# Performance work log

Measured on AMD Instinct MI355X. Metric: run time of the kernel, lower is better.

Reference implementation:

```python
import jax, jax.numpy as jnp
import numpy as np

B, S, D, H = 8, 1024, 512, 8


def setup_inputs() -> dict:
    key = jax.random.key(0)
    ks = jax.random.split(key, 10)
    sc = 0.05
    return {
        "x": jax.random.normal(ks[0], (B, S, D), dtype=jnp.float32),
        "Wq": jax.random.normal(ks[1], (H, D, D), dtype=jnp.float32) * sc,
        "bq": jax.random.normal(ks[2], (H, D), dtype=jnp.float32) * sc,
        "Wk": jax.random.normal(ks[3], (H, D, D), dtype=jnp.float32) * sc,
        "bk": jax.random.normal(ks[4], (H, D), dtype=jnp.float32) * sc,
        "Wv": jax.random.normal(ks[5], (H, D, D), dtype=jnp.float32) * sc,
        "bv": jax.random.normal(ks[6], (H, D), dtype=jnp.float32) * sc,
        "Wo": jax.random.normal(ks[7], (H * D, D), dtype=jnp.float32) * sc,
        "bo": jax.random.normal(ks[8], (D,), dtype=jnp.float32) * sc,
    }


def reference(x, Wq, bq, Wk, bk, Wv, bv, Wo, bo):
    # Per-head full-dim projections, batched across heads.
    # x: [B,S,D]; Wq/Wk/Wv: [H,D,D]; b*: [H,D]
    q = jnp.einsum('bsd,hde->bhse', x, Wq) + bq[None, :, None, :]
    k = jnp.einsum('bsd,hde->bhse', x, Wk) + bk[None, :, None, :]
    v = jnp.einsum('bsd,hde->bhse', x, Wv) + bv[None, :, None, :]
    d = x.shape[-1]
    scores = jnp.einsum('bhse,bhte->bhst', q, k) / jnp.sqrt(jnp.float32(d))
    attn = jax.nn.softmax(scores, axis=-1)
    heads = jnp.einsum('bhst,bhte->bhse', attn, v)  # [B,H,S,D]
    # concat along feature dim (head order matches torch cat order)
    concat = jnp.transpose(heads, (0, 2, 1, 3)).reshape(x.shape[0], x.shape[1], -1)
    return concat @ Wo + bo
```

## Files before the change

kernel.cpp:

```cpp
#include <hip/hip_runtime.h>
#include <cstdint>
#include <cstddef>

#define BB 8
#define SS 1024
#define DDIM 512
#define HH 8
#define BS 8192
#define HD 4096

typedef __attribute__((ext_vector_type(4))) float f32x4;
typedef __attribute__((ext_vector_type(8))) short bf16x8;
typedef __attribute__((ext_vector_type(4))) unsigned short u16x4;


__device__ __forceinline__ unsigned short f2bf(float f) {
  union { float f; unsigned int u; } x; x.f = f;
  unsigned int r = x.u + 0x7fffu + ((x.u >> 16) & 1u);
  return (unsigned short)(r >> 16);
}

__device__ __forceinline__ void gload16(const void* g, void* l) {
  __builtin_amdgcn_global_load_lds(
      (const __attribute__((address_space(1))) unsigned int*)g,
      (__attribute__((address_space(3))) unsigned int*)l, 16, 0, 0);
}

#define BAR_LGKM() do { asm volatile("s_waitcnt lgkmcnt(0)" ::: "memory"); \
                        __builtin_amdgcn_s_barrier(); } while (0)
#define BAR_ALL()  do { asm volatile("s_waitcnt vmcnt(0) lgkmcnt(0)" ::: "memory"); \
                        __builtin_amdgcn_s_barrier(); } while (0)


__global__ void k_convert(const float* __restrict__ in, unsigned short* __restrict__ out, int n4) {
  int i = blockIdx.x * blockDim.x + threadIdx.x;
  if (i < n4) {
    float4 v = ((const float4*)in)[i];
    u16x4 o;
    o[0] = f2bf(v.x); o[1] = f2bf(v.y); o[2] = f2bf(v.z); o[3] = f2bf(v.w);
    ((u16x4*)out)[i] = o;
  }
}

__global__ void k_transpose_f2b(const float* __restrict__ in, unsigned short* __restrict__ out,
                                int R, int C) {
  __shared__ unsigned short tile[64][65];
  const int z = blockIdx.z;
  const int r0 = blockIdx.x << 6, c0 = blockIdx.y << 6;
  const float* ip = in + (size_t)z * R * C;
  unsigned short* op = out + (size_t)z * R * C;
  const int t = threadIdx.x;
#pragma unroll
  for (int i = 0; i < 16; ++i) {
    int idx = t + (i << 8); int r = idx >> 6, c = idx & 63;
    tile[r][c] = f2bf(ip[(size_t)(r0 + r) * C + (c0 + c)]);
  }
  __syncthreads();
#pragma unroll
  for (int i = 0; i < 16; ++i) {
    int idx = t + (i << 8); int c = idx >> 6, r = idx & 63;
    op[(size_t)(c0 + c) * R + (r0 + r)] = tile[r][c];
  }
}

__global__ void k_transpose_b2b(const unsigned short* __restrict__ in,
                                unsigned short* __restrict__ out, int R, int C) {
  __shared__ unsigned short tile[64][65];
  const int z = blockIdx.z;
  const int r0 = blockIdx.x << 6, c0 = blockIdx.y << 6;
  const unsigned short* ip = in + (size_t)z * R * C;
  unsigned short* op = out + (size_t)z * R * C;
  const int t = threadIdx.x;
#pragma unroll
  for (int i = 0; i < 16; ++i) {
    int idx = t + (i << 8); int r = idx >> 6, c = idx & 63;
    tile[r][c] = ip[(size_t)(r0 + r) * C + (c0 + c)];
  }
  __syncthreads();
#pragma unroll
  for (int i = 0; i < 16; ++i) {
    int idx = t + (i << 8); int c = idx >> 6, r = idx & 63;
    op[(size_t)(c0 + c) * R + (r0 + r)] = tile[r][c];
  }
}

template<int A_RS, int B_RS, int KITERS>
__device__ __forceinline__ void gemm_core(const char* Ag, const char* Bg,
                                          char* As, char* Bs, f32x4 acc[4][4]) {
  const int tid = threadIdx.x;
  const int wave = tid >> 6, lane = tid & 63;
  const int wr = (wave >> 1) << 6, wc = (wave & 1) << 6;
  const int srow = (wave << 3) + (lane >> 3);
  const int scol = ((lane & 7) << 4) ^ ((lane >> 3) << 4);

  for (int kb = 0; kb < KITERS; ++kb) {
    __syncthreads();
#pragma unroll
    for (int j = 0; j < 4; ++j) {
      gload16(Ag + (size_t)(j * 32 + srow) * A_RS + (size_t)kb * 128 + scol,
              As + j * 4096 + wave * 1024);
      gload16(Bg + (size_t)(j * 32 + srow) * B_RS + (size_t)kb * 128 + scol,
              Bs + j * 4096 + wave * 1024);
    }
    asm volatile("s_waitcnt vmcnt(0)" ::: "memory");
    __syncthreads();
#pragma unroll
    for (int ks = 0; ks < 2; ++ks) {
      bf16x8 af[4], bfr[4];
      const int kcol = (ks << 6) + ((lane >> 4) << 4);
#pragma unroll
      for (int i = 0; i < 4; ++i) {
        const int ar = wr + (i << 4) + (lane & 15);
        af[i] = *(const bf16x8*)(As + ar * 128 + (kcol ^ ((ar & 7) << 4)));
        const int br = wc + (i << 4) + (lane & 15);
        bfr[i] = *(const bf16x8*)(Bs + br * 128 + (kcol ^ ((br & 7) << 4)));
      }
#pragma unroll
      for (int i = 0; i < 4; ++i)
#pragma unroll
        for (int j = 0; j < 4; ++j)
          acc[i][j] = __builtin_amdgcn_mfma_f32_16x16x32_bf16(af[i], bfr[j], acc[i][j], 0, 0, 0);
    }
  }
}

__global__ __launch_bounds__(256, 2) void k_gemm_qkv(
    const unsigned short* __restrict__ xbf,
    const unsigned short* __restrict__ wqT, const unsigned short* __restrict__ wkT,
    const unsigned short* __restrict__ wvT,
    const float* __restrict__ bq, const float* __restrict__ bk, const float* __restrict__ bv,
    unsigned short* __restrict__ Qo, unsigned short* __restrict__ Ko,
    unsigned short* __restrict__ Vo, int b0) {
  __shared__ __align__(16) char As[16384], Bs[16384];
  const int z = blockIdx.z;
  const int p = z >> 3, h = z & 7;
  const unsigned short* wT = (p == 0) ? wqT : (p == 1) ? wkT : wvT;
  const float* bias = ((p == 0) ? bq : (p == 1) ? bk : bv) + (h << 9);
  unsigned short* dst = (p == 0) ? Qo : (p == 1) ? Ko : Vo;
  const int m0 = blockIdx.x << 7, n0 = blockIdx.y << 7;
  const char* Ag = (const char*)xbf + ((size_t)(b0 << 10) + m0) * 1024;
  const char* Bg = (const char*)wT + (size_t)h * 524288 + (size_t)n0 * 1024;
  f32x4 acc[4][4] = {};
  gemm_core<1024, 1024, 8>(Ag, Bg, As, Bs, acc);

  const int tid = threadIdx.x, wave = tid >> 6, lane = tid & 63;
  const int wr = (wave >> 1) << 6, wc = (wave & 1) << 6;
#pragma unroll
  for (int j = 0; j < 4; ++j) {
    const int col = n0 + wc + (j << 4) + (lane & 15);
    const float bb = bias[col];
#pragma unroll
    for (int i = 0; i < 4; ++i)
#pragma unroll
      for (int r = 0; r < 4; ++r) {
        const int m = m0 + wr + (i << 4) + ((lane >> 4) << 2) + r;
        const int lb = m >> 10, s = m & 1023;
        dst[((size_t)((lb * HH + h) * SS + s) << 9) + col] = f2bf(acc[i][j][r] + bb);
      }
  }
}

__global__ __launch_bounds__(256, 2) void k_gemm_out(
    const unsigned short* __restrict__ concat, const unsigned short* __restrict__ woT,
    const float* __restrict__ bo, float* __restrict__ out) {
  __shared__ __align__(16) char As[16384], Bs[16384];
  const int m0 = blockIdx.x << 7, n0 = blockIdx.y << 7;
  const char* Ag = (const char*)concat + (size_t)m0 * 8192;
  const char* Bg = (const char*)woT + (size_t)n0 * 8192;
  f32x4 acc[4][4] = {};
  gemm_core<8192, 8192, 64>(Ag, Bg, As, Bs, acc);

  const int tid = threadIdx.x, wave = tid >> 6, lane = tid & 63;
  const int wr = (wave >> 1) << 6, wc = (wave & 1) << 6;
#pragma unroll
  for (int j = 0; j < 4; ++j) {
    const int col = n0 + wc + (j << 4) + (lane & 15);
    const float bb = bo[col];
#pragma unroll
    for (int i = 0; i < 4; ++i)
#pragma unroll
      for (int r = 0; r < 4; ++r) {
        const int m = m0 + wr + (i << 4) + ((lane >> 4) << 2) + r;
        out[(size_t)m * DDIM + col] = acc[i][j][r] + bb;
      }
  }
}

__global__ __launch_bounds__(256, 2) void k_attn(
    const unsigned short* __restrict__ Qg, const unsigned short* __restrict__ Kg,
    const unsigned short* __restrict__ VTg, unsigned short* __restrict__ Og,
    int b0, int bhMask, int bhShift) {
  __shared__ __align__(16) char smem[73088];
  char* Ksm = smem;
  char* Vsm = smem + 32768;
  float* Ssm = (float*)(smem + 65536);
  char* Psm = smem + 70144;
  float* msm = (float*)(smem + 72704);
  float* lsm = (float*)(smem + 72832);
  float* fsm = (float*)(smem + 72960);

  const int tid = threadIdx.x, wave = tid >> 6, lane = tid & 63;
  const int qt = blockIdx.x >> bhShift;
  const int bh = blockIdx.x & bhMask;
  const int q0 = qt << 5;
  const char* Qb = (const char*)Qg + (size_t)bh * (SS * DDIM * 2);
  const char* Kb = (const char*)Kg + (size_t)bh * (SS * DDIM * 2);
  const char* Vb = (const char*)VTg + (size_t)bh * (SS * DDIM * 2);

  const int qi = wave >> 1, ni = wave & 1;

  if (tid < 32) { msm[tid] = -1e30f; lsm[tid] = 0.0f; }

#pragma unroll
  for (int j = 0; j < 8; ++j) {
    const int row = (j << 2) + wave;
    gload16(Qb + (size_t)(q0 + row) * 1024 + ((lane << 4) ^ ((row & 7) << 4)),
            Ksm + row * 1024);
  }
  BAR_ALL();
  bf16x8 qf[16];
  {
    const int qrow = (qi << 4) + (lane & 15);
    const int qswz = (qrow & 7) << 4;
    const int kg = (lane >> 4) << 4;
#pragma unroll
    for (int ks = 0; ks < 16; ++ks)
      qf[ks] = *(const bf16x8*)(Ksm + qrow * 1024 + (((ks << 6) + kg) ^ qswz));
  }
  BAR_LGKM();

#define STAGE_K(KV0)                                                           \
  {                                                                            \
    _Pragma("unroll")                                                          \
    for (int j = 0; j < 8; ++j) {                                              \
      const int row = (j << 2) + wave;                                         \
      gload16(Kb + (size_t)((KV0) + row) * 1024 + ((lane << 4) ^ ((row & 7) << 4)), \
              Ksm + row * 1024);                                               \
    }                                                                          \
  }
#define STAGE_V(KV0)                                                           \
  {                                                                            \
    _Pragma("unroll")                                                          \
    for (int j = 0; j < 8; ++j) {                                              \
      const int idx = (j << 2) + wave;                                         \
      const int dr = (idx << 4) + (lane >> 2);                                 \
      gload16(Vb + (size_t)dr * 2048 + (size_t)((KV0) << 1) +                  \
                  (((lane & 3) << 4) ^ (((lane >> 2) & 3) << 4)),              \
              Vsm + idx * 1024);                                               \
    }                                                                          \
  }

  STAGE_K(0);
  STAGE_V(0);

  f32x4 accO[2][8] = {};
  const float scale = 0.044194173824159216f;

  for (int kt = 0; kt < 32; ++kt) {
    const int kvn = (kt + 1) << 5;
    BAR_ALL();

    f32x4 a0 = {}, a1 = {};
    {
      const int krow = (ni << 4) + (lane & 15);
      const char* kb2 = Ksm + krow * 1024;
      const int ksz = (krow & 7) << 4;
      const int kg = (lane >> 4) << 4;
      __builtin_amdgcn_s_setprio(1);
#pragma unroll
      for (int ks = 0; ks < 16; ks += 2) {
        const bf16x8 k0 = *(const bf16x8*)(kb2 + (((ks << 6) + kg) ^ ksz));
        const bf16x8 k1 = *(const bf16x8*)(kb2 + ((((ks + 1) << 6) + kg) ^ ksz));
        a0 = __builtin_amdgcn_mfma_f32_16x16x32_bf16(qf[ks], k0, a0, 0, 0, 0);
        a1 = __builtin_amdgcn_mfma_f32_16x16x32_bf16(qf[ks + 1], k1, a1, 0, 0, 0);
      }
      __builtin_amdgcn_s_setprio(0);
    }
    {
      const int srow = (qi << 4) + ((lane >> 4) << 2);
      const int scol = (ni << 4) + (lane & 15);
#pragma unroll
      for (int r = 0; r < 4; ++r) Ssm[(srow + r) * 36 + scol] = a0[r] + a1[r];
    }
    BAR_LGKM();

    if (kt != 31) STAGE_K(kvn);

    {
      const int row = tid >> 3, c8 = tid & 7;
      f32x4 sv = *(const f32x4*)(Ssm + row * 36 + (c8 << 2));
#pragma unroll
      for (int c = 0; c < 4; ++c) sv[c] *= scale;
      float mx = fmaxf(fmaxf(sv[0], sv[1]), fmaxf(sv[2], sv[3]));
      mx = fmaxf(mx, __shfl_xor(mx, 1));
      mx = fmaxf(mx, __shfl_xor(mx, 2));
      mx = fmaxf(mx, __shfl_xor(mx, 4));
      const float mold = msm[row];
      const float mnew = fmaxf(mold, mx);
      const float fac = __expf(mold - mnew);
      float ls = 0.0f;
      u16x4 pv;
#pragma unroll
      for (int c = 0; c < 4; ++c) {
        const float p = __expf(sv[c] - mnew);
        ls += p;
        pv[c] = f2bf(p);
      }
      ls += __shfl_xor(ls, 1);
      ls += __shfl_xor(ls, 2);
      ls += __shfl_xor(ls, 4);
      if ((tid & 7) == 0) {
        msm[row] = mnew;
        lsm[row] = lsm[row] * fac + ls;
        fsm[row] = fac;
      }
      *(u16x4*)(Psm + row * 80 + (c8 << 3)) = pv;
    }
    BAR_LGKM();

    {
      float facs[2][4];
      bf16x8 pf[2], vf[8];
      const int rb = (lane >> 4) << 2;
      const int kg = (lane >> 4) << 4;
#pragma unroll
      for (int i = 0; i < 2; ++i) {
#pragma unroll
        for (int r = 0; r < 4; ++r) facs[i][r] = fsm[(i << 4) + rb + r];
        const int pr = (i << 4) + (lane & 15);
        pf[i] = *(const bf16x8*)(Psm + pr * 80 + kg);
      }
#pragma unroll
      for (int j = 0; j < 8; ++j) {
        const int vr = (wave << 7) + (j << 4) + (lane & 15);
        vf[j] = *(const bf16x8*)(Vsm + vr * 64 + (kg ^ ((vr & 3) << 4)));
      }
      BAR_LGKM();

      if (kt != 31) STAGE_V(kvn);

#pragma unroll
      for (int i = 0; i < 2; ++i)
#pragma unroll
        for (int j = 0; j < 8; ++j)
#pragma unroll
          for (int r = 0; r < 4; ++r) accO[i][j][r] *= facs[i][r];
      __builtin_amdgcn_s_setprio(1);
#pragma unroll
      for (int i = 0; i < 2; ++i)
#pragma unroll
        for (int j = 0; j < 8; ++j)
          accO[i][j] = __builtin_amdgcn_mfma_f32_16x16x32_bf16(pf[i], vf[j], accO[i][j], 0, 0, 0);
      __builtin_amdgcn_s_setprio(0);
    }
  }

  {
    const int b = b0 + (bh >> 3), h = bh & 7;
    const int rb = (lane >> 4) << 2;
    float linv[2][4];
#pragma unroll
    for (int i = 0; i < 2; ++i)
#pragma unroll
      for (int r = 0; r < 4; ++r) linv[i][r] = 1.0f / lsm[(i << 4) + rb + r];
#pragma unroll
    for (int i = 0; i < 2; ++i)
#pragma unroll
      for (int j = 0; j < 8; ++j) {
        const int col = (wave << 7) + (j << 4) + (lane & 15);
#pragma unroll
        for (int r = 0; r < 4; ++r) {
          const int s = q0 + (i << 4) + rb + r;
          Og[((size_t)((b << 10) + s)) * HD + (h << 9) + col] = f2bf(accO[i][j][r] * linv[i][r]);
        }
      }
  }
#undef STAGE_K
#undef STAGE_V
}


extern "C" void kernel_launch(void* const* d_in, const int* in_sizes, int n_in,
                              void* d_out, int out_size, void* d_ws, size_t ws_size,
                              hipStream_t stream) {
  const float* x  = (const float*)d_in[0];
  const float* Wq = (const float*)d_in[1];
  const float* bq = (const float*)d_in[2];
  const float* Wk = (const float*)d_in[3];
  const float* bk = (const float*)d_in[4];
  const float* Wv = (const float*)d_in[5];
  const float* bv = (const float*)d_in[6];
  const float* Wo = (const float*)d_in[7];
  const float* bo = (const float*)d_in[8];
  float* out = (float*)d_out;
  char* ws = (char*)d_ws;

  unsigned short* xbf = (unsigned short*)(ws);
  unsigned short* wqT = (unsigned short*)(ws + 8388608);
  unsigned short* wkT = (unsigned short*)(ws + 12582912);
  unsigned short* wvT = (unsigned short*)(ws + 16777216);
  unsigned short* woT = (unsigned short*)(ws + 20971520);
  unsigned short* Cw  = (unsigned short*)(ws + 25165824);
  const size_t pbase = 25165824ull + 67108864ull;

  int nb = 1;
  if (ws_size >= pbase + 4ull * 8ull * 8388608ull) nb = 8;
  else if (ws_size >= pbase + 4ull * 2ull * 8388608ull) nb = 2;
  const size_t pb = (size_t)nb * 8388608ull;
  unsigned short* Qp  = (unsigned short*)(ws + pbase);
  unsigned short* Kp  = (unsigned short*)(ws + pbase + pb);
  unsigned short* Vp  = (unsigned short*)(ws + pbase + 2 * pb);
  unsigned short* VTp = (unsigned short*)(ws + pbase + 3 * pb);

  k_convert<<<4096, 256, 0, stream>>>(x, xbf, BS * DDIM / 4);
  k_transpose_f2b<<<dim3(8, 8, 8), 256, 0, stream>>>(Wq, wqT, 512, 512);
  k_transpose_f2b<<<dim3(8, 8, 8), 256, 0, stream>>>(Wk, wkT, 512, 512);
  k_transpose_f2b<<<dim3(8, 8, 8), 256, 0, stream>>>(Wv, wvT, 512, 512);
  k_transpose_f2b<<<dim3(64, 8, 1), 256, 0, stream>>>(Wo, woT, 4096, 512);

  const int bhShift = (nb == 8) ? 6 : (nb == 2) ? 4 : 3;
  const int bhMask = (8 * nb) - 1;
  for (int b0 = 0; b0 < BB; b0 += nb) {
    k_gemm_qkv<<<dim3(8 * nb, 4, 24), 256, 0, stream>>>(xbf, wqT, wkT, wvT,
                                                        bq, bk, bv, Qp, Kp, Vp, b0);
    k_transpose_b2b<<<dim3(16, 8, 8 * nb), 256, 0, stream>>>(Vp, VTp, SS, DDIM);
    k_attn<<<dim3(32 << bhShift), 256, 0, stream>>>(Qp, Kp, VTp, Cw, b0, bhMask, bhShift);
  }

  k_gemm_out<<<dim3(64, 4), 256, 0, stream>>>(Cw, woT, bo, out);
}
```

Before: 689.5 us.

## Double-buffer K/V tiles in attention kernel and launch per batch

The attention kernel now double-buffers K and V tiles in LDS (about 135 KB), issuing the next tile's loads at the top of each iteration so they overlap the current QK and PV MFMAs, which removes the mid-iteration barrier before V staging. QK accumulation uses four independent accumulators, and the score buffer stride changes from 36 to 33. The host now launches one 256-block attention grid per batch instead of one large grid. The larger LDS footprint drops occupancy to one block per CU, and the smaller grids add launch overhead and may underfill the device.

```diff
diff --git a/kernel.cpp b/kernel.cpp
--- a/kernel.cpp
+++ b/kernel.cpp
@@ -186,59 +186,41 @@
   }
 }
 
-__global__ __launch_bounds__(256, 2) void k_attn(
+__global__ __launch_bounds__(256, 1) void k_attn(
     const unsigned short* __restrict__ Qg, const unsigned short* __restrict__ Kg,
     const unsigned short* __restrict__ VTg, unsigned short* __restrict__ Og,
-    int b0, int bhMask, int bhShift) {
-  __shared__ __align__(16) char smem[73088];
-  char* Ksm = smem;
-  char* Vsm = smem + 32768;
-  float* Ssm = (float*)(smem + 65536);
-  char* Psm = smem + 70144;
-  float* msm = (float*)(smem + 72704);
-  float* lsm = (float*)(smem + 72832);
-  float* fsm = (float*)(smem + 72960);
+    int gb, int lb) {
+  __shared__ __align__(16) char smem[138240];
+  float* Ssm = (float*)(smem + 131072);
+  char* Psm = smem + 135296;
+  float* msm = (float*)(smem + 137856);
+  float* lsm = (float*)(smem + 137984);
+  float* fsm = (float*)(smem + 138112);
 
   const int tid = threadIdx.x, wave = tid >> 6, lane = tid & 63;
-  const int qt = blockIdx.x >> bhShift;
-  const int bh = blockIdx.x & bhMask;
+  const int qt = blockIdx.x >> 3;
+  const int h  = blockIdx.x & 7;
+  const int bh = (lb << 3) + h;
   const int q0 = qt << 5;
   const char* Qb = (const char*)Qg + (size_t)bh * (SS * DDIM * 2);
   const char* Kb = (const char*)Kg + (size_t)bh * (SS * DDIM * 2);
   const char* Vb = (const char*)VTg + (size_t)bh * (SS * DDIM * 2);
 
   const int qi = wave >> 1, ni = wave & 1;
+  const int kg16 = (lane >> 4) << 4;
 
   if (tid < 32) { msm[tid] = -1e30f; lsm[tid] = 0.0f; }
 
-#pragma unroll
-  for (int j = 0; j < 8; ++j) {
-    const int row = (j << 2) + wave;
-    gload16(Qb + (size_t)(q0 + row) * 1024 + ((lane << 4) ^ ((row & 7) << 4)),
-            Ksm + row * 1024);
-  }
-  BAR_ALL();
-  bf16x8 qf[16];
-  {
-    const int qrow = (qi << 4) + (lane & 15);
-    const int qswz = (qrow & 7) << 4;
-    const int kg = (lane >> 4) << 4;
-#pragma unroll
-    for (int ks = 0; ks < 16; ++ks)
-      qf[ks] = *(const bf16x8*)(Ksm + qrow * 1024 + (((ks << 6) + kg) ^ qswz));
-  }
-  BAR_LGKM();
-
-#define STAGE_K(KV0)                                                           \
+#define STAGE_K(KV0, BUF)                                                      \
   {                                                                            \
     _Pragma("unroll")                                                          \
     for (int j = 0; j < 8; ++j) {                                              \
       const int row = (j << 2) + wave;                                         \
       gload16(Kb + (size_t)((KV0) + row) * 1024 + ((lane << 4) ^ ((row & 7) << 4)), \
-              Ksm + row * 1024);                                               \
+              smem + (BUF) * 32768 + row * 1024);                              \
     }                                                                          \
   }
-#define STAGE_V(KV0)                                                           \
+#define STAGE_V(KV0, BUF)                                                      \
   {                                                                            \
     _Pragma("unroll")                                                          \
     for (int j = 0; j < 8; ++j) {                                              \
@@ -246,51 +228,70 @@
       const int dr = (idx << 4) + (lane >> 2);                                 \
       gload16(Vb + (size_t)dr * 2048 + (size_t)((KV0) << 1) +                  \
                   (((lane & 3) << 4) ^ (((lane >> 2) & 3) << 4)),              \
-              Vsm + idx * 1024);                                               \
+              smem + 65536 + (BUF) * 32768 + idx * 1024);                      \
     }                                                                          \
   }
 
-  STAGE_K(0);
-  STAGE_V(0);
+#pragma unroll
+  for (int j = 0; j < 8; ++j) {
+    const int row = (j << 2) + wave;
+    gload16(Qb + (size_t)(q0 + row) * 1024 + ((lane << 4) ^ ((row & 7) << 4)),
+            smem + 32768 + row * 1024);
+  }
+  BAR_ALL();
+  bf16x8 qf[16];
+  {
+    const int qrow = (qi << 4) + (lane & 15);
+    const int qswz = (qrow & 7) << 4;
+#pragma unroll
+    for (int ks = 0; ks < 16; ++ks)
+      qf[ks] = *(const bf16x8*)(smem + 32768 + qrow * 1024 + (((ks << 6) + kg16) ^ qswz));
+  }
+  STAGE_K(0, 0);
+  STAGE_V(0, 0);
 
   f32x4 accO[2][8] = {};
   const float scale = 0.044194173824159216f;
 
   for (int kt = 0; kt < 32; ++kt) {
-    const int kvn = (kt + 1) << 5;
+    const int cur = kt & 1;
     BAR_ALL();
-
-    f32x4 a0 = {}, a1 = {};
+    if (kt != 31) {
+      STAGE_K((kt + 1) << 5, cur ^ 1);
+      STAGE_V((kt + 1) << 5, cur ^ 1);
+    }
+
     {
+      f32x4 a0 = {}, a1 = {}, a2 = {}, a3 = {};
       const int krow = (ni << 4) + (lane & 15);
-      const char* kb2 = Ksm + krow * 1024;
+      const char* kb2 = smem + cur * 32768 + krow * 1024;
       const int ksz = (krow & 7) << 4;
-      const int kg = (lane >> 4) << 4;
       __builtin_amdgcn_s_setprio(1);
 #pragma unroll
-      for (int ks = 0; ks < 16; ks += 2) {
-        const bf16x8 k0 = *(const bf16x8*)(kb2 + (((ks << 6) + kg) ^ ksz));
-        const bf16x8 k1 = *(const bf16x8*)(kb2 + ((((ks + 1) << 6) + kg) ^ ksz));
-        a0 = __builtin_amdgcn_mfma_f32_16x16x32_bf16(qf[ks], k0, a0, 0, 0, 0);
+      for (int ks = 0; ks < 16; ks += 4) {
+        const bf16x8 k0 = *(const bf16x8*)(kb2 + ((((ks + 0) << 6) + kg16) ^ ksz));
+        const bf16x8 k1 = *(const bf16x8*)(kb2 + ((((ks + 1) << 6) + kg16) ^ ksz));
+        const bf16x8 k2 = *(const bf16x8*)(kb2 + ((((ks + 2) << 6) + kg16) ^ ksz));
+        const bf16x8 k3 = *(const bf16x8*)(kb2 + ((((ks + 3) << 6) + kg16) ^ ksz));
+        a0 = __builtin_amdgcn_mfma_f32_16x16x32_bf16(qf[ks + 0], k0, a0, 0, 0, 0);
         a1 = __builtin_amdgcn_mfma_f32_16x16x32_bf16(qf[ks + 1], k1, a1, 0, 0, 0);
+        a2 = __builtin_amdgcn_mfma_f32_16x16x32_bf16(qf[ks + 2], k2, a2, 0, 0, 0);
+        a3 = __builtin_amdgcn_mfma_f32_16x16x32_bf16(qf[ks + 3], k3, a3, 0, 0, 0);
       }
       __builtin_amdgcn_s_setprio(0);
-    }
-    {
+      const f32x4 s = (a0 + a1) + (a2 + a3);
       const int srow = (qi << 4) + ((lane >> 4) << 2);
       const int scol = (ni << 4) + (lane & 15);
 #pragma unroll
-      for (int r = 0; r < 4; ++r) Ssm[(srow + r) * 36 + scol] = a0[r] + a1[r];
+      for (int r = 0; r < 4; ++r) Ssm[(srow + r) * 33 + scol] = s[r];
     }
     BAR_LGKM();
-
-    if (kt != 31) STAGE_K(kvn);
 
     {
       const int row = tid >> 3, c8 = tid & 7;
-      f32x4 sv = *(const f32x4*)(Ssm + row * 36 + (c8 << 2));
-#pragma unroll
-      for (int c = 0; c < 4; ++c) sv[c] *= scale;
+      float sv[4];
+#pragma unroll
+      for (int c = 0; c < 4; ++c) sv[c] = Ssm[row * 33 + (c8 << 2) + c] * scale;
       float mx = fmaxf(fmaxf(sv[0], sv[1]), fmaxf(sv[2], sv[3]));
       mx = fmaxf(mx, __shfl_xor(mx, 1));
       mx = fmaxf(mx, __shfl_xor(mx, 2));
@@ -322,23 +323,19 @@
       float facs[2][4];
       bf16x8 pf[2], vf[8];
       const int rb = (lane >> 4) << 2;
-      const int kg = (lane >> 4) << 4;
+      const char* vb2 = smem + 65536 + cur * 32768;
 #pragma unroll
       for (int i = 0; i < 2; ++i) {
 #pragma unroll
         for (int r = 0; r < 4; ++r) facs[i][r] = fsm[(i << 4) + rb + r];
         const int pr = (i << 4) + (lane & 15);
-        pf[i] = *(const bf16x8*)(Psm + pr * 80 + kg);
+        pf[i] = *(const bf16x8*)(Psm + pr * 80 + kg16);
       }
 #pragma unroll
       for (int j = 0; j < 8; ++j) {
         const int vr = (wave << 7) + (j << 4) + (lane & 15);
-        vf[j] = *(const bf16x8*)(Vsm + vr * 64 + (kg ^ ((vr & 3) << 4)));
-      }
-      BAR_LGKM();
-
-      if (kt != 31) STAGE_V(kvn);
-
+        vf[j] = *(const bf16x8*)(vb2 + vr * 64 + (kg16 ^ ((vr & 3) << 4)));
+      }
 #pragma unroll
       for (int i = 0; i < 2; ++i)
 #pragma unroll
@@ -356,7 +353,6 @@
   }
 
   {
-    const int b = b0 + (bh >> 3), h = bh & 7;
     const int rb = (lane >> 4) << 2;
     float linv[2][4];
 #pragma unroll
@@ -371,7 +367,7 @@
 #pragma unroll
         for (int r = 0; r < 4; ++r) {
           const int s = q0 + (i << 4) + rb + r;
-          Og[((size_t)((b << 10) + s)) * HD + (h << 9) + col] = f2bf(accO[i][j][r] * linv[i][r]);
+          Og[((size_t)((gb << 10) + s)) * HD + (h << 9) + col] = f2bf(accO[i][j][r] * linv[i][r]);
         }
       }
   }
@@ -418,13 +414,12 @@
   k_transpose_f2b<<<dim3(8, 8, 8), 256, 0, stream>>>(Wv, wvT, 512, 512);
   k_transpose_f2b<<<dim3(64, 8, 1), 256, 0, stream>>>(Wo, woT, 4096, 512);
 
-  const int bhShift = (nb == 8) ? 6 : (nb == 2) ? 4 : 3;
-  const int bhMask = (8 * nb) - 1;
   for (int b0 = 0; b0 < BB; b0 += nb) {
     k_gemm_qkv<<<dim3(8 * nb, 4, 24), 256, 0, stream>>>(xbf, wqT, wkT, wvT,
                                                         bq, bk, bv, Qp, Kp, Vp, b0);
     k_transpose_b2b<<<dim3(16, 8, 8 * nb), 256, 0, stream>>>(Vp, VTp, SS, DDIM);
-    k_attn<<<dim3(32 << bhShift), 256, 0, stream>>>(Qp, Kp, VTp, Cw, b0, bhMask, bhShift);
+    for (int bb = 0; bb < nb; ++bb)
+      k_attn<<<dim3(256), 256, 0, stream>>>(Qp, Kp, VTp, Cw, b0 + bb, bb);
   }
 
   k_gemm_out<<<dim3(64, 4), 256, 0, stream>>>(Cw, woT, bo, out);
```

After: 876.7 us. +27.2%, slower.
